# Optimization experiments

Hardware: AMD Instinct MI355X
Metric: run time of the kernel (lower is better)

Reference implementation:

```python
import jax, jax.numpy as jnp
import numpy as np

D = 128
NUM_STRUCTURES = 8
N = 1024
BERNOULLI_INIT = 0.5


def setup_inputs() -> dict:
    key = jax.random.key(0)
    k_x, k_m, k_w = jax.random.split(key, 3)
    x = jax.random.normal(k_x, (N, D), dtype=jnp.float32)
    # maskings: 0/1 DAG masks (one per structure), float for multiplication
    maskings = jax.random.randint(k_m, (NUM_STRUCTURES, D, D), 0, 2).astype(jnp.float32)
    # Bernoulli logits/probs theta, initialized at bernouilli_init
    theta = jnp.full((NUM_STRUCTURES, D, D), BERNOULLI_INIT, dtype=jnp.float32)
    # Linear structural-equation weights
    W = jax.random.normal(k_w, (NUM_STRUCTURES, D, D), dtype=jnp.float32)
    return {"x": x, "maskings": maskings, "theta": theta, "W": W}


def _bernoulli_ste(theta):
    # BernoulliSTERoot: hard Bernoulli sample with straight-through estimator.
    # Fixed noise key for deterministic reference.
    u = jax.random.uniform(jax.random.key(42), theta.shape, dtype=theta.dtype)
    hard = (u < theta).astype(theta.dtype)
    return theta + jax.lax.stop_gradient(hard - theta)


def reference(x, maskings, theta, W):
    # dags[o,p,c]: masked Bernoulli sample of edge p->c for structure o
    dags = maskings * _bernoulli_ste(theta)  # (o, d, d)
    # masked_x[o,n,c,p] = dags[o,p,c] * x[n,p]  (large 4-D intermediate, as in original)
    masked_x = jnp.einsum('opc,np->oncp', dags, x)  # (o, n, d, d)
    # x_hat[o,n,c] = sum_p masked_x[o,n,c,p] * W[o,p,c]
    x_hat = jnp.einsum('oncp,opc->onc', masked_x, W)  # (o, n, d)
    return x_hat
```

## Files before the change

### kernel.cpp

```cpp
#include <hip/hip_runtime.h>
#include <stdint.h>

#define NSTRUCT 8
#define NROWS   1024
#define DD      128


__device__ __forceinline__ uint32_t rotl32(uint32_t x, uint32_t d) {
  return (x << d) | (x >> (32u - d));
}

__device__ __forceinline__ uint32_t threefry_bits(uint32_t i) {
  const uint32_t ks0 = 0u;
  const uint32_t ks1 = 42u;
  const uint32_t ks2 = 0x1BD11BDAu ^ ks0 ^ ks1;
  uint32_t x0 = 0u + ks0;
  uint32_t x1 = i  + ks1;
#define TF_RND(r) { x0 += x1; x1 = rotl32(x1, r); x1 ^= x0; }
  TF_RND(13) TF_RND(15) TF_RND(26) TF_RND(6)
  x0 += ks1; x1 += ks2 + 1u;
  TF_RND(17) TF_RND(29) TF_RND(16) TF_RND(24)
  x0 += ks2; x1 += ks0 + 2u;
  TF_RND(13) TF_RND(15) TF_RND(26) TF_RND(6)
  x0 += ks0; x1 += ks1 + 3u;
  TF_RND(17) TF_RND(29) TF_RND(16) TF_RND(24)
  x0 += ks1; x1 += ks2 + 4u;
  TF_RND(13) TF_RND(15) TF_RND(26) TF_RND(6)
  x0 += ks2; x1 += ks0 + 5u;
#undef TF_RND
  return x0 ^ x1;
}

__global__ __launch_bounds__(256, 1) void nnl0_fused(
    const float* __restrict__ x,
    const float* __restrict__ maskings,
    const float* __restrict__ theta,
    const float* __restrict__ W,
    float* __restrict__ out) {
  __shared__ float Ms[DD * 32];
  __shared__ float xs[DD * DD];

  const int b   = blockIdx.x;
  const int o   = b >> 5;
  const int cq  = (b >> 3) & 3;
  const int rt  = b & 7;
  const int n0  = rt << 7;
  const int cb  = cq << 5;
  const int tid = threadIdx.x;

  {
    const int mbase = o * DD * DD;
#pragma unroll 2
    for (int k = 0; k < 16; ++k) {
      int idx = k * 256 + tid;
      int p = idx >> 5;
      int c = idx & 31;
      int gi = mbase + p * DD + cb + c;
      uint32_t bits = threefry_bits((uint32_t)gi);
      float u = __uint_as_float((bits >> 9) | 0x3f800000u) - 1.0f;
      float v = (u < theta[gi]) ? maskings[gi] * W[gi] : 0.0f;
      Ms[p * 32 + c] = v;
    }
  }

#pragma unroll 2
  for (int k = 0; k < 16; ++k) {
    int q = k * 256 + tid;
    int n = q >> 5;
    int pc = (q & 31) << 2;
    float4 v = *(const float4*)&x[(size_t)(n0 + n) * DD + pc];
    int g = n >> 2, nj = n & 3;
    xs[(pc + 0) * DD + ((g ^ ((pc + 0) & 31)) << 2) + nj] = v.x;
    xs[(pc + 1) * DD + ((g ^ ((pc + 1) & 31)) << 2) + nj] = v.y;
    xs[(pc + 2) * DD + ((g ^ ((pc + 2) & 31)) << 2) + nj] = v.z;
    xs[(pc + 3) * DD + ((g ^ ((pc + 3) & 31)) << 2) + nj] = v.w;
  }

  __syncthreads();

  const int c0 = (tid & 7) << 2;
  const int g  = tid >> 3;

  float acc[4][4];
#pragma unroll
  for (int a = 0; a < 4; ++a)
#pragma unroll
    for (int bb = 0; bb < 4; ++bb) acc[a][bb] = 0.0f;

#pragma unroll 4
  for (int p = 0; p < DD; ++p) {
    float4 bv = *(const float4*)&Ms[p * 32 + c0];
    float4 av = *(const float4*)&xs[p * DD + ((g ^ (p & 31)) << 2)];
    acc[0][0] += av.x * bv.x; acc[0][1] += av.x * bv.y; acc[0][2] += av.x * bv.z; acc[0][3] += av.x * bv.w;
    acc[1][0] += av.y * bv.x; acc[1][1] += av.y * bv.y; acc[1][2] += av.y * bv.z; acc[1][3] += av.y * bv.w;
    acc[2][0] += av.z * bv.x; acc[2][1] += av.z * bv.y; acc[2][2] += av.z * bv.z; acc[2][3] += av.z * bv.w;
    acc[3][0] += av.w * bv.x; acc[3][1] += av.w * bv.y; acc[3][2] += av.w * bv.z; acc[3][3] += av.w * bv.w;
  }

  float* obase = out + ((size_t)o * NROWS + n0 + g * 4) * DD + cb + c0;
#pragma unroll
  for (int j = 0; j < 4; ++j) {
    *(float4*)&obase[(size_t)j * DD] =
        make_float4(acc[j][0], acc[j][1], acc[j][2], acc[j][3]);
  }
}

extern "C" void kernel_launch(void* const* d_in, const int* in_sizes, int n_in,
                              void* d_out, int out_size, void* d_ws, size_t ws_size,
                              hipStream_t stream) {
  const float* x        = (const float*)d_in[0];
  const float* maskings = (const float*)d_in[1];
  const float* theta    = (const float*)d_in[2];
  const float* W        = (const float*)d_in[3];
  float* out = (float*)d_out;

  nnl0_fused<<<NSTRUCT * 4 * 8, 256, 0, stream>>>(x, maskings, theta, W, out);
}
```

Baseline: 78.09 us.

## Compute masked GEMM with bf16 MFMA and restructure block tiling

```diff
diff --git a/kernel.cpp b/kernel.cpp
--- a/kernel.cpp
+++ b/kernel.cpp
@@ -5,6 +5,8 @@
 #define NROWS   1024
 #define DD      128
 
+typedef short bf16x8 __attribute__((ext_vector_type(8)));
+typedef float f32x4  __attribute__((ext_vector_type(4)));
 
 __device__ __forceinline__ uint32_t rotl32(uint32_t x, uint32_t d) {
   return (x << d) | (x >> (32u - d));
@@ -31,79 +33,81 @@
   return x0 ^ x1;
 }
 
-__global__ __launch_bounds__(256, 1) void nnl0_fused(
+__device__ __forceinline__ uint16_t f32_to_bf16_rne(float v) {
+  uint32_t fb = __float_as_uint(v);
+  uint32_t lsb = (fb >> 16) & 1u;
+  return (uint16_t)((fb + 0x7fffu + lsb) >> 16);
+}
+
+__device__ __forceinline__ uint32_t pk_bf16_trunc(float lo, float hi) {
+  return __builtin_amdgcn_perm(__float_as_uint(hi), __float_as_uint(lo),
+                               0x07060302u);
+}
+
+__global__ __launch_bounds__(512, 1) void nnl0_fused(
     const float* __restrict__ x,
     const float* __restrict__ maskings,
     const float* __restrict__ theta,
     const float* __restrict__ W,
     float* __restrict__ out) {
-  __shared__ float Ms[DD * 32];
-  __shared__ float xs[DD * DD];
+  __shared__ uint16_t Bf[2048];
 
   const int b   = blockIdx.x;
-  const int o   = b >> 5;
-  const int cq  = (b >> 3) & 3;
-  const int rt  = b & 7;
-  const int n0  = rt << 7;
-  const int cb  = cq << 5;
+  const int o   = b >> 3;
+  const int ct  = b & 7;
   const int tid = threadIdx.x;
+  const int w    = tid >> 6;
+  const int lane = tid & 63;
 
-  {
-    const int mbase = o * DD * DD;
-#pragma unroll 2
-    for (int k = 0; k < 16; ++k) {
-      int idx = k * 256 + tid;
-      int p = idx >> 5;
-      int c = idx & 31;
-      int gi = mbase + p * DD + cb + c;
-      uint32_t bits = threefry_bits((uint32_t)gi);
-      float u = __uint_as_float((bits >> 9) | 0x3f800000u) - 1.0f;
-      float v = (u < theta[gi]) ? maskings[gi] * W[gi] : 0.0f;
-      Ms[p * 32 + c] = v;
-    }
+#pragma unroll
+  for (int s = 0; s < 4; ++s) {
+    int f    = s * 512 + tid;
+    int j    = f & 7;
+    int lf   = (f >> 3) & 63;
+    int kk   = f >> 9;
+    int p    = kk * 32 + ((lf >> 4) << 3) + j;
+    int c    = (ct << 4) + (lf & 15);
+    int gi   = (o << 14) + (p << 7) + c;
+    uint32_t bits = threefry_bits((uint32_t)gi);
+    float u = __uint_as_float((bits >> 9) | 0x3f800000u) - 1.0f;
+    float v = (u < theta[gi]) ? maskings[gi] * W[gi] : 0.0f;
+    Bf[f] = f32_to_bf16_rne(v);
   }
-
-#pragma unroll 2
-  for (int k = 0; k < 16; ++k) {
-    int q = k * 256 + tid;
-    int n = q >> 5;
-    int pc = (q & 31) << 2;
-    float4 v = *(const float4*)&x[(size_t)(n0 + n) * DD + pc];
-    int g = n >> 2, nj = n & 3;
-    xs[(pc + 0) * DD + ((g ^ ((pc + 0) & 31)) << 2) + nj] = v.x;
-    xs[(pc + 1) * DD + ((g ^ ((pc + 1) & 31)) << 2) + nj] = v.y;
-    xs[(pc + 2) * DD + ((g ^ ((pc + 2) & 31)) << 2) + nj] = v.z;
-    xs[(pc + 3) * DD + ((g ^ ((pc + 3) & 31)) << 2) + nj] = v.w;
-  }
-
   __syncthreads();
 
-  const int c0 = (tid & 7) << 2;
-  const int g  = tid >> 3;
+  const bf16x8* bfv = (const bf16x8*)Bf;
+  bf16x8 bfrag[4];
+#pragma unroll
+  for (int kk = 0; kk < 4; ++kk) bfrag[kk] = bfv[kk * 64 + lane];
 
-  float acc[4][4];
+  const int kq   = (lane >> 4) << 3;
+  const int mloc = lane & 15;
+  const int rq   = (lane >> 4) << 2;
+
 #pragma unroll
-  for (int a = 0; a < 4; ++a)
+  for (int i = 0; i < 8; ++i) {
+    const int nb = (w << 7) + (i << 4);
+    const float* xr = x + (size_t)(nb + mloc) * DD + kq;
+
+    f32x4 acc = {0.f, 0.f, 0.f, 0.f};
 #pragma unroll
-    for (int bb = 0; bb < 4; ++bb) acc[a][bb] = 0.0f;
+    for (int kk = 0; kk < 4; ++kk) {
+      float4 q0 = *(const float4*)(xr + kk * 32);
+      float4 q1 = *(const float4*)(xr + kk * 32 + 4);
+      union { bf16x8 v; uint32_t u[4]; } af;
+      af.u[0] = pk_bf16_trunc(q0.x, q0.y);
+      af.u[1] = pk_bf16_trunc(q0.z, q0.w);
+      af.u[2] = pk_bf16_trunc(q1.x, q1.y);
+      af.u[3] = pk_bf16_trunc(q1.z, q1.w);
+      acc = __builtin_amdgcn_mfma_f32_16x16x32_bf16(af.v, bfrag[kk], acc, 0, 0, 0);
+    }
 
-#pragma unroll 4
-  for (int p = 0; p < DD; ++p) {
-    float4 bv = *(const float4*)&Ms[p * 32 + c0];
-    float4 av = *(const float4*)&xs[p * DD + ((g ^ (p & 31)) << 2)];
-    acc[0][0] += av.x * bv.x; acc[0][1] += av.x * bv.y; acc[0][2] += av.x * bv.z; acc[0][3] += av.x * bv.w;
-    acc[1][0] += av.y * bv.x; acc[1][1] += av.y * bv.y; acc[1][2] += av.y * bv.z; acc[1][3] += av.y * bv.w;
-    acc[2][0] += av.z * bv.x; acc[2][1] += av.z * bv.y; acc[2][2] += av.z * bv.z; acc[2][3] += av.z * bv.w;
-    acc[3][0] += av.w * bv.x; acc[3][1] += av.w * bv.y; acc[3][2] += av.w * bv.z; acc[3][3] += av.w * bv.w;
-  }
-
-  float* obase = out + ((size_t)o * NROWS + n0 + g * 4) * DD + cb + c0;
+    float* obase = out + ((size_t)o * NROWS + nb + rq) * DD + (ct << 4) + mloc;
 #pragma unroll
-  for (int j = 0; j < 4; ++j) {
-    *(float4*)&obase[(size_t)j * DD] =
-        make_float4(acc[j][0], acc[j][1], acc[j][2], acc[j][3]);
+    for (int r = 0; r < 4; ++r) obase[(size_t)r * DD] = acc[r];
   }
 }
+
 
 extern "C" void kernel_launch(void* const* d_in, const int* in_sizes, int n_in,
                               void* d_out, int out_size, void* d_ws, size_t ws_size,
@@ -114,5 +118,5 @@
   const float* W        = (const float*)d_in[3];
   float* out = (float*)d_out;
 
-  nnl0_fused<<<NSTRUCT * 4 * 8, 256, 0, stream>>>(x, maskings, theta, W, out);
+  nnl0_fused<<<NSTRUCT * 8, 512, 0, stream>>>(x, maskings, theta, W, out);
 }
```

New measurement: 77.68 us. No clear change (-0.5%).
